# Performance work log

Hardware: AMD Instinct MI355X
Metric: run time of the kernel (lower is better)

Reference implementation:

```python
import jax, jax.numpy as jnp
import numpy as np

B, T, C = 4, 2048, 1024
H = 16
HD = C // H  # 64


def setup_inputs() -> dict:
    key = jax.random.key(0)
    ks = jax.random.split(key, 4)
    x = jax.random.normal(ks[0], (B, T, C), dtype=jnp.float32)
    # c_attn: Linear(C, 3C, bias=False)  (qkv_bias=False)
    w_attn = jax.random.normal(ks[1], (C, 3 * C), dtype=jnp.float32) / np.sqrt(C)
    # c_proj: Linear(C, C) with bias (nn.Linear default)
    w_proj = jax.random.normal(ks[2], (C, C), dtype=jnp.float32) / np.sqrt(C)
    b_proj = jax.random.normal(ks[3], (C,), dtype=jnp.float32) * 0.01
    return {"x": x, "w_attn": w_attn, "w_proj": w_proj, "b_proj": b_proj}


def reference(x, w_attn, w_proj, b_proj):
    b, t, c = x.shape
    qkv = x @ w_attn  # [B,T,3C]
    q, k, v = jnp.split(qkv, 3, axis=-1)
    # [B,H,T,HD]
    q = q.reshape(b, t, H, HD).transpose(0, 2, 1, 3)
    k = k.reshape(b, t, H, HD).transpose(0, 2, 1, 3)
    v = v.reshape(b, t, H, HD).transpose(0, 2, 1, 3)
    scale = 1.0 / np.sqrt(HD)
    attn = jnp.einsum('bhqd,bhkd->bhqk', q, k) * scale  # [B,H,T,T]
    causal = jnp.tril(jnp.ones((t, t), dtype=bool))
    attn = jnp.where(causal, attn, -jnp.inf)
    attn = jax.nn.softmax(attn, axis=-1)
    out = jnp.einsum('bhqk,bhkd->bhqd', attn, v)  # [B,H,T,HD]
    out = out.transpose(0, 2, 1, 3).reshape(b, t, c)
    return out @ w_proj + b_proj
```

## Files before the change

kernel.cpp:

```cpp
#include <hip/hip_runtime.h>

#define BB 4
#define TT 2048
#define CC 1024
#define C3 3072
#define HH 16
#define HD 64
#define BT 8192

#define TS 32
#define TSZ (64 * TS)

typedef __bf16 bf16x8 __attribute__((ext_vector_type(8)));
typedef float floatx4 __attribute__((ext_vector_type(4)));
typedef unsigned uintx2 __attribute__((ext_vector_type(2)));
typedef unsigned short u16;

__device__ __forceinline__ u16 f2bf(float f) {
  union { float f; unsigned u; } a; a.f = f;
  return (u16)((a.u + 0x7fffu + ((a.u >> 16) & 1u)) >> 16);
}
__device__ __forceinline__ bf16x8 ld8(const u16* p) { return *(const bf16x8*)p; }
__device__ __forceinline__ floatx4 mfma16(bf16x8 a, bf16x8 b, floatx4 c) {
  return __builtin_amdgcn_mfma_f32_16x16x32_bf16(a, b, c, 0, 0, 0);
}

__device__ __forceinline__ void gload16(const u16* g, u16* l) {
  __builtin_amdgcn_global_load_lds(
      (const __attribute__((address_space(1))) void*)g,
      (__attribute__((address_space(3))) void*)l, 16, 0, 0);
}

__device__ __forceinline__ void qd_xchg(unsigned a, unsigned b,
                                        unsigned& r0, unsigned& r1) {
  uintx2 t = __builtin_amdgcn_permlane32_swap(a, b, false, false);
  uintx2 r = __builtin_amdgcn_permlane16_swap(t[0], t[1], false, false);
  r0 = r[0]; r1 = r[1];
}

__global__ __launch_bounds__(256) void tobf16_kernel(const float4* __restrict__ src,
                                                     ushort4* __restrict__ dst, int n4) {
  int i = blockIdx.x * 256 + threadIdx.x;
  if (i >= n4) return;
  float4 v = src[i];
  ushort4 o; o.x = f2bf(v.x); o.y = f2bf(v.y); o.z = f2bf(v.z); o.w = f2bf(v.w);
  dst[i] = o;
}

__global__ __launch_bounds__(256) void transpose_bf16_kernel(const float* __restrict__ src,
                                                             u16* __restrict__ dst,
                                                             int K, int N) {
  __shared__ float s[64][65];
  const int t = threadIdx.x;
  const int r = t >> 4;
  const int c = (t & 15) * 4;
  const int k0 = blockIdx.y * 64, n0 = blockIdx.x * 64;
#pragma unroll
  for (int i = 0; i < 4; ++i) {
    float4 v = *(const float4*)&src[(size_t)(k0 + r + i * 16) * N + n0 + c];
    s[r + i * 16][c + 0] = v.x; s[r + i * 16][c + 1] = v.y;
    s[r + i * 16][c + 2] = v.z; s[r + i * 16][c + 3] = v.w;
  }
  __syncthreads();
#pragma unroll
  for (int i = 0; i < 4; ++i) {
    const int nn = r + i * 16;
    ushort4 o;
    o.x = f2bf(s[c + 0][nn]); o.y = f2bf(s[c + 1][nn]);
    o.z = f2bf(s[c + 2][nn]); o.w = f2bf(s[c + 3][nn]);
    *(ushort4*)&dst[(size_t)(n0 + nn) * K + k0 + c] = o;
  }
}

template<int MODE>
__global__ __launch_bounds__(256) void gemm_kernel(
    const u16* __restrict__ A, const u16* __restrict__ B,
    const float* __restrict__ bias, float* __restrict__ outf,
    u16* __restrict__ qk, u16* __restrict__ vT,
    int M, int N, int K) {
  __shared__ u16 smem[2][2][2 * TSZ];

  const int t = threadIdx.x;
  const int w = t >> 6, lane = t & 63, lr = lane & 15, qd = lane >> 4;
  const int wm = w >> 1, wn = w & 1;
  const int m0 = blockIdx.y * 128, n0 = blockIdx.x * 128;

  const int sr = t >> 2;
  const int sc = (t & 3) * 8;
  const int wb = (t & ~63) * 8;
  const u16* Ag = A + (size_t)(m0 + sr) * K + sc;
  const u16* Bg = B + (size_t)(n0 + sr) * K + sc;

  floatx4 acc[4][4] = {};

  {
    u16* sA = &smem[0][0][0];
    u16* sB = &smem[0][1][0];
    gload16(Ag,                  &sA[wb]);
    gload16(Ag + (size_t)64 * K, &sA[TSZ + wb]);
    gload16(Bg,                  &sB[wb]);
    gload16(Bg + (size_t)64 * K, &sB[TSZ + wb]);
  }
  __syncthreads();

  for (int k0 = 0; k0 < K; k0 += 32) {
    const int p = (k0 >> 5) & 1;
    if (k0 + 32 < K) {
      u16* sA = &smem[p ^ 1][0][0];
      u16* sB = &smem[p ^ 1][1][0];
      gload16(Ag + k0 + 32,                  &sA[wb]);
      gload16(Ag + (size_t)64 * K + k0 + 32, &sA[TSZ + wb]);
      gload16(Bg + k0 + 32,                  &sB[wb]);
      gload16(Bg + (size_t)64 * K + k0 + 32, &sB[TSZ + wb]);
    }
    const u16* sA = &smem[p][0][0];
    const u16* sB = &smem[p][1][0];

    bf16x8 af[4], bf[4];
#pragma unroll
    for (int mj = 0; mj < 4; ++mj) af[mj] = ld8(&sA[(wm * 64 + mj * 16 + lr) * TS + qd * 8]);
#pragma unroll
    for (int nj = 0; nj < 4; ++nj) bf[nj] = ld8(&sB[(wn * 64 + nj * 16 + lr) * TS + qd * 8]);
#pragma unroll
    for (int mj = 0; mj < 4; ++mj)
#pragma unroll
      for (int nj = 0; nj < 4; ++nj)
        acc[mj][nj] = mfma16(af[mj], bf[nj], acc[mj][nj]);
    __syncthreads();
  }

  const int rowg0 = m0 + wm * 64;
  const int colg0 = n0 + wn * 64;
  if constexpr (MODE == 2) {
#pragma unroll
    for (int nj = 0; nj < 4; ++nj) {
      const int col = colg0 + nj * 16 + lr;
      const float bv = bias[col];
#pragma unroll
      for (int mj = 0; mj < 4; ++mj)
#pragma unroll
        for (int i = 0; i < 4; ++i)
          outf[(size_t)(rowg0 + mj * 16 + qd * 4 + i) * N + col] = acc[mj][nj][i] + bv;
    }
  } else {
    u16* Tw = &smem[0][0][0] + w * (32 * 72);
    const bool isV = (n0 >= 2 * CC);
    if (!isV) {
      const float qs = (n0 < CC) ? 0.18033688011f : 1.0f;
#pragma unroll
      for (int half = 0; half < 2; ++half) {
#pragma unroll
        for (int m2 = 0; m2 < 2; ++m2)
#pragma unroll
          for (int nj = 0; nj < 4; ++nj)
#pragma unroll
            for (int i = 0; i < 4; ++i)
              Tw[(m2 * 16 + qd * 4 + i) * 72 + nj * 16 + lr] =
                  f2bf(acc[half * 2 + m2][nj][i] * qs);
#pragma unroll
        for (int s = 0; s < 4; ++s) {
          const int rl = s * 8 + (lane >> 3);
          const int c0 = (lane & 7) * 8;
          *(bf16x8*)&qk[(size_t)(rowg0 + half * 32 + rl) * (2 * CC) + colg0 + c0] =
              ld8(&Tw[rl * 72 + c0]);
        }
      }
    } else {
      const int bI = m0 >> 11;
      const int tbase = (m0 & (TT - 1)) + wm * 64;
      const int dim0 = colg0 - 2 * CC;
#pragma unroll
      for (int half = 0; half < 2; ++half) {
#pragma unroll
        for (int n2 = 0; n2 < 2; ++n2)
#pragma unroll
          for (int mj = 0; mj < 4; ++mj)
#pragma unroll
            for (int i = 0; i < 4; ++i)
              Tw[(n2 * 16 + lr) * 72 + mj * 16 + qd * 4 + i] =
                  f2bf(acc[mj][half * 2 + n2][i]);
#pragma unroll
        for (int s = 0; s < 4; ++s) {
          const int dl = s * 8 + (lane >> 3);
          const int t0 = (lane & 7) * 8;
          *(bf16x8*)&vT[((size_t)(bI << 10) + dim0 + half * 32 + dl) * TT + tbase + t0] =
              ld8(&Tw[dl * 72 + t0]);
        }
      }
    }
  }
}

__global__ __launch_bounds__(256, 5) void attn_kernel(const u16* __restrict__ qk,
                                                      const u16* __restrict__ vT,
                                                      u16* __restrict__ att) {
  __shared__ u16 sKV[2][4][TSZ];

  const int t = threadIdx.x;
  const int w = t >> 6, lane = t & 63, lr = lane & 15, qd = lane >> 4;
  const int qtile = 31 - blockIdx.y;
  const int bh = blockIdx.x;
  const int b = bh >> 4, h = bh & 15;
  const int q0 = qtile * 64;
  const u16* qbase = qk + (size_t)b * TT * (2 * CC);

  const u16* qp = qbase + (size_t)(q0 + w * 16 + lr) * (2 * CC) + h * HD;
  const bf16x8 qf0 = ld8(qp + qd * 8);
  const bf16x8 qf1 = ld8(qp + 32 + qd * 8);

  const int sr = t >> 2, sc = (t & 3) * 8;
  const int wb = (t & ~63) * 8;
  const u16* Kg = qbase + (size_t)sr * (2 * CC) + CC + h * HD + sc;
  const u16* Vg = vT + ((size_t)bh * HD + sr) * TT + sc;

  float lsum = 0.f;
  floatx4 o[4] = {};
  const int myq = q0 + w * 16 + lr;

  {
    u16* b0 = &sKV[0][0][0];
    gload16(Kg,      &b0[wb]);
    gload16(Kg + 32, &b0[TSZ + wb]);
    gload16(Vg,      &b0[2 * TSZ + wb]);
    gload16(Vg + 32, &b0[3 * TSZ + wb]);
  }
  __syncthreads();

  for (int kt = 0; kt <= qtile; ++kt) {
    if (kt < qtile) {
      const int kn = (kt + 1) * 64;
      u16* bn = &sKV[(kt + 1) & 1][0][0];
      gload16(Kg + (size_t)kn * (2 * CC),      &bn[wb]);
      gload16(Kg + (size_t)kn * (2 * CC) + 32, &bn[TSZ + wb]);
      gload16(Vg + kn,                         &bn[2 * TSZ + wb]);
      gload16(Vg + kn + 32,                    &bn[3 * TSZ + wb]);
    }

    const u16* sK0 = &sKV[kt & 1][0][0];
    const u16* sK1 = &sKV[kt & 1][1][0];
    const u16* sV0 = &sKV[kt & 1][2][0];
    const u16* sV1 = &sKV[kt & 1][3][0];

    floatx4 s[4] = {};
#pragma unroll
    for (int j = 0; j < 4; ++j) {
      bf16x8 kf0 = ld8(&sK0[(j * 16 + lr) * TS + qd * 8]);
      bf16x8 kf1 = ld8(&sK1[(j * 16 + lr) * TS + qd * 8]);
      s[j] = mfma16(kf0, qf0, s[j]);
      s[j] = mfma16(kf1, qf1, s[j]);
    }

    const bool diag = (kt == qtile);
    unsigned W[4][2];
#pragma unroll
    for (int j = 0; j < 4; ++j) {
      float p[4];
#pragma unroll
      for (int i = 0; i < 4; ++i) {
        p[i] = __builtin_amdgcn_exp2f(s[j][i]);
        if (diag) {
          const int key = kt * 64 + j * 16 + qd * 4 + i;
          p[i] = (key <= myq) ? p[i] : 0.f;
        }
        lsum += p[i];
      }
      W[j][0] = __builtin_amdgcn_perm(__float_as_uint(p[1]), __float_as_uint(p[0]), 0x07060302);
      W[j][1] = __builtin_amdgcn_perm(__float_as_uint(p[3]), __float_as_uint(p[2]), 0x07060302);
    }

    uint4 F0, F1;
    qd_xchg(W[0][0], W[1][0], F0.x, F0.z);
    qd_xchg(W[0][1], W[1][1], F0.y, F0.w);
    qd_xchg(W[2][0], W[3][0], F1.x, F1.z);
    qd_xchg(W[2][1], W[3][1], F1.y, F1.w);
    const bf16x8 pf0 = __builtin_bit_cast(bf16x8, F0);
    const bf16x8 pf1 = __builtin_bit_cast(bf16x8, F1);

#pragma unroll
    for (int j = 0; j < 4; ++j) {
      bf16x8 vf0 = ld8(&sV0[(j * 16 + lr) * TS + qd * 8]);
      bf16x8 vf1 = ld8(&sV1[(j * 16 + lr) * TS + qd * 8]);
      o[j] = mfma16(pf0, vf0, o[j]);
      o[j] = mfma16(pf1, vf1, o[j]);
    }
    __syncthreads();
  }

  lsum += __shfl_xor(lsum, 16);
  lsum += __shfl_xor(lsum, 32);
  float linv[4];
#pragma unroll
  for (int i = 0; i < 4; ++i) linv[i] = 1.0f / __shfl(lsum, qd * 4 + i);

#pragma unroll
  for (int j = 0; j < 4; ++j)
#pragma unroll
    for (int i = 0; i < 4; ++i) {
      const size_t row = (size_t)b * TT + q0 + w * 16 + qd * 4 + i;
      att[row * CC + h * HD + j * 16 + lr] = f2bf(o[j][i] * linv[i]);
    }
}

extern "C" void kernel_launch(void* const* d_in, const int* in_sizes, int n_in,
                              void* d_out, int out_size, void* d_ws, size_t ws_size,
                              hipStream_t stream) {
  const float* x      = (const float*)d_in[0];
  const float* w_attn = (const float*)d_in[1];
  const float* w_proj = (const float*)d_in[2];
  const float* b_proj = (const float*)d_in[3];
  float* out = (float*)d_out;

  char* ws = (char*)d_ws;
  u16* xb  = (u16*)(ws + 0);
  u16* waT = (u16*)(ws + 16777216);
  u16* wpT = (u16*)(ws + 23068672);
  u16* qk  = (u16*)(ws + 25165824);
  u16* vT  = (u16*)(ws + 58720256);
  u16* att = (u16*)(ws + 75497472);

  tobf16_kernel<<<8192, 256, 0, stream>>>((const float4*)x, (ushort4*)xb, 2097152);
  transpose_bf16_kernel<<<dim3(48, 16), 256, 0, stream>>>(w_attn, waT, CC, C3);
  transpose_bf16_kernel<<<dim3(16, 16), 256, 0, stream>>>(w_proj, wpT, CC, CC);

  gemm_kernel<1><<<dim3(24, 64), 256, 0, stream>>>(xb, waT, nullptr, nullptr, qk, vT,
                                                   BT, C3, CC);
  attn_kernel<<<dim3(64, 32), 256, 0, stream>>>(qk, vT, att);

  gemm_kernel<2><<<dim3(8, 64), 256, 0, stream>>>(att, wpT, b_proj, out, nullptr, nullptr,
                                                  BT, CC, CC);
}
```

Before: 236.2 us.

## Split attention key tile across warp pairs and reduce partial outputs in LDS

Each warp now handles 32 query rows and half of each 64-key tile, instead of 16 query rows and the full tile. K and V fragments loaded from shared memory are therefore reused across two query subtiles, which cuts LDS reads per MFMA. The partial outputs and row sums from the two key halves are combined through shared memory in a final reduction. The cost is more registers (launch bounds drop to 4 blocks per SM) plus one extra sync and LDS round trip at the end.

```diff
diff --git a/kernel.cpp b/kernel.cpp
--- a/kernel.cpp
+++ b/kernel.cpp
@@ -191,31 +191,39 @@
   }
 }
 
-__global__ __launch_bounds__(256, 5) void attn_kernel(const u16* __restrict__ qk,
+__global__ __launch_bounds__(256, 4) void attn_kernel(const u16* __restrict__ qk,
                                                       const u16* __restrict__ vT,
                                                       u16* __restrict__ att) {
   __shared__ u16 sKV[2][4][TSZ];
 
   const int t = threadIdx.x;
   const int w = t >> 6, lane = t & 63, lr = lane & 15, qd = lane >> 4;
+  const int m2 = w >> 1;
+  const int ks = w & 1;
   const int qtile = 31 - blockIdx.y;
   const int bh = blockIdx.x;
   const int b = bh >> 4, h = bh & 15;
   const int q0 = qtile * 64;
   const u16* qbase = qk + (size_t)b * TT * (2 * CC);
 
-  const u16* qp = qbase + (size_t)(q0 + w * 16 + lr) * (2 * CC) + h * HD;
-  const bf16x8 qf0 = ld8(qp + qd * 8);
-  const bf16x8 qf1 = ld8(qp + 32 + qd * 8);
+  bf16x8 qf[2][2];
+  int myq[2];
+#pragma unroll
+  for (int ms = 0; ms < 2; ++ms) {
+    const int qrow = q0 + m2 * 32 + ms * 16 + lr;
+    myq[ms] = qrow;
+    const u16* qp = qbase + (size_t)qrow * (2 * CC) + h * HD;
+    qf[ms][0] = ld8(qp + qd * 8);
+    qf[ms][1] = ld8(qp + 32 + qd * 8);
+  }
 
   const int sr = t >> 2, sc = (t & 3) * 8;
   const int wb = (t & ~63) * 8;
   const u16* Kg = qbase + (size_t)sr * (2 * CC) + CC + h * HD + sc;
   const u16* Vg = vT + ((size_t)bh * HD + sr) * TT + sc;
 
-  float lsum = 0.f;
-  floatx4 o[4] = {};
-  const int myq = q0 + w * 16 + lr;
+  float lsum[2] = {0.f, 0.f};
+  floatx4 o[2][4] = {};
 
   {
     u16* b0 = &sKV[0][0][0];
@@ -238,67 +246,99 @@
 
     const u16* sK0 = &sKV[kt & 1][0][0];
     const u16* sK1 = &sKV[kt & 1][1][0];
-    const u16* sV0 = &sKV[kt & 1][2][0];
-    const u16* sV1 = &sKV[kt & 1][3][0];
-
-    floatx4 s[4] = {};
+    const u16* sVk = &sKV[kt & 1][2 + ks][0];
+
+    floatx4 s[2][2] = {};
+#pragma unroll
+    for (int ku = 0; ku < 2; ++ku) {
+      const int krow = ks * 32 + ku * 16 + lr;
+      bf16x8 kf0 = ld8(&sK0[krow * TS + qd * 8]);
+      bf16x8 kf1 = ld8(&sK1[krow * TS + qd * 8]);
+#pragma unroll
+      for (int ms = 0; ms < 2; ++ms) {
+        s[ms][ku] = mfma16(kf0, qf[ms][0], s[ms][ku]);
+        s[ms][ku] = mfma16(kf1, qf[ms][1], s[ms][ku]);
+      }
+    }
+
+    const bool diag = (kt == qtile);
+    uint4 F[2];
+#pragma unroll
+    for (int ms = 0; ms < 2; ++ms) {
+      unsigned W[2][2];
+#pragma unroll
+      for (int ku = 0; ku < 2; ++ku) {
+        float p[4];
+#pragma unroll
+        for (int i = 0; i < 4; ++i) {
+          p[i] = __builtin_amdgcn_exp2f(s[ms][ku][i]);
+          if (diag) {
+            const int key = kt * 64 + ks * 32 + ku * 16 + qd * 4 + i;
+            p[i] = (key <= myq[ms]) ? p[i] : 0.f;
+          }
+          lsum[ms] += p[i];
+        }
+        W[ku][0] = __builtin_amdgcn_perm(__float_as_uint(p[1]), __float_as_uint(p[0]), 0x07060302);
+        W[ku][1] = __builtin_amdgcn_perm(__float_as_uint(p[3]), __float_as_uint(p[2]), 0x07060302);
+      }
+      qd_xchg(W[0][0], W[1][0], F[ms].x, F[ms].z);
+      qd_xchg(W[0][1], W[1][1], F[ms].y, F[ms].w);
+    }
+    const bf16x8 pf0 = __builtin_bit_cast(bf16x8, F[0]);
+    const bf16x8 pf1 = __builtin_bit_cast(bf16x8, F[1]);
+
 #pragma unroll
     for (int j = 0; j < 4; ++j) {
-      bf16x8 kf0 = ld8(&sK0[(j * 16 + lr) * TS + qd * 8]);
-      bf16x8 kf1 = ld8(&sK1[(j * 16 + lr) * TS + qd * 8]);
-      s[j] = mfma16(kf0, qf0, s[j]);
-      s[j] = mfma16(kf1, qf1, s[j]);
-    }
-
-    const bool diag = (kt == qtile);
-    unsigned W[4][2];
-#pragma unroll
-    for (int j = 0; j < 4; ++j) {
-      float p[4];
-#pragma unroll
-      for (int i = 0; i < 4; ++i) {
-        p[i] = __builtin_amdgcn_exp2f(s[j][i]);
-        if (diag) {
-          const int key = kt * 64 + j * 16 + qd * 4 + i;
-          p[i] = (key <= myq) ? p[i] : 0.f;
+      bf16x8 vf = ld8(&sVk[(j * 16 + lr) * TS + qd * 8]);
+      o[0][j] = mfma16(pf0, vf, o[0][j]);
+      o[1][j] = mfma16(pf1, vf, o[1][j]);
+    }
+    __syncthreads();
+  }
+
+#pragma unroll
+  for (int ms = 0; ms < 2; ++ms) {
+    lsum[ms] += __shfl_xor(lsum[ms], 16);
+    lsum[ms] += __shfl_xor(lsum[ms], 32);
+  }
+
+  float* sO = (float*)&sKV[0][0][0];
+  float* sL = (float*)((char*)&sKV[0][0][0] + 17408);
+
+  if (qd == 0) {
+    sL[w * 32 + lr]      = lsum[0];
+    sL[w * 32 + 16 + lr] = lsum[1];
+  }
+  if (ks == 1) {
+#pragma unroll
+    for (int ms = 0; ms < 2; ++ms)
+#pragma unroll
+      for (int j = 0; j < 4; ++j)
+#pragma unroll
+        for (int i = 0; i < 4; ++i)
+          sO[(m2 * 32 + ms * 16 + qd * 4 + i) * 68 + j * 16 + lr] = o[ms][j][i];
+  }
+  __syncthreads();
+
+  if (ks == 0) {
+    const int pw = w + 1;
+#pragma unroll
+    for (int ms = 0; ms < 2; ++ms) {
+      const float lt = lsum[ms] + sL[pw * 32 + ms * 16 + lr];
+      float linv[4];
+#pragma unroll
+      for (int i = 0; i < 4; ++i) linv[i] = 1.0f / __shfl(lt, qd * 4 + i);
+#pragma unroll
+      for (int j = 0; j < 4; ++j)
+#pragma unroll
+        for (int i = 0; i < 4; ++i) {
+          const float ov = o[ms][j][i] +
+              sO[(m2 * 32 + ms * 16 + qd * 4 + i) * 68 + j * 16 + lr];
+          const size_t row = (size_t)b * TT + q0 + m2 * 32 + ms * 16 + qd * 4 + i;
+          att[row * CC + h * HD + j * 16 + lr] = f2bf(ov * linv[i]);
         }
-        lsum += p[i];
-      }
-      W[j][0] = __builtin_amdgcn_perm(__float_as_uint(p[1]), __float_as_uint(p[0]), 0x07060302);
-      W[j][1] = __builtin_amdgcn_perm(__float_as_uint(p[3]), __float_as_uint(p[2]), 0x07060302);
-    }
-
-    uint4 F0, F1;
-    qd_xchg(W[0][0], W[1][0], F0.x, F0.z);
-    qd_xchg(W[0][1], W[1][1], F0.y, F0.w);
-    qd_xchg(W[2][0], W[3][0], F1.x, F1.z);
-    qd_xchg(W[2][1], W[3][1], F1.y, F1.w);
-    const bf16x8 pf0 = __builtin_bit_cast(bf16x8, F0);
-    const bf16x8 pf1 = __builtin_bit_cast(bf16x8, F1);
-
-#pragma unroll
-    for (int j = 0; j < 4; ++j) {
-      bf16x8 vf0 = ld8(&sV0[(j * 16 + lr) * TS + qd * 8]);
-      bf16x8 vf1 = ld8(&sV1[(j * 16 + lr) * TS + qd * 8]);
-      o[j] = mfma16(pf0, vf0, o[j]);
-      o[j] = mfma16(pf1, vf1, o[j]);
-    }
-    __syncthreads();
-  }
-
-  lsum += __shfl_xor(lsum, 16);
-  lsum += __shfl_xor(lsum, 32);
-  float linv[4];
-#pragma unroll
-  for (int i = 0; i < 4; ++i) linv[i] = 1.0f / __shfl(lsum, qd * 4 + i);
-
-#pragma unroll
-  for (int j = 0; j < 4; ++j)
-#pragma unroll
-    for (int i = 0; i < 4; ++i) {
-      const size_t row = (size_t)b * TT + q0 + w * 16 + qd * 4 + i;
-      att[row * CC + h * HD + j * 16 + lr] = f2bf(o[j][i] * linv[i]);
-    }
+    }
+  }
 }
 
 extern "C" void kernel_launch(void* const* d_in, const int* in_sizes, int n_in,
```

After: 237.9 us. No clear change (+0.7%).

## Replace QKV GEMM with 256x256-tile 8-wave kernel using swizzled LDS pipeline

Applied to the files above, without the earlier changes.

Adds a new QKV projection GEMM that gives each 512-thread block a 256x256 output tile with K-step 64. It uses XOR-swizzled LDS staging through direct global-to-LDS loads, and a hand-scheduled eight-phase loop that interleaves loads for later K tiles with MFMA phases, gated by vmcnt waits and raw barriers. The larger tile raises data reuse per byte loaded and is meant to hide memory latency, with setprio favouring the MFMA bursts. The cost is more accumulator registers and a fragile manual schedule that hard-codes K=1024 (8 iterations of 2 K-tiles). The old MODE 1 path is removed from the generic GEMM, which now only serves the output projection.

```diff
diff --git a/kernel.cpp b/kernel.cpp
--- a/kernel.cpp
+++ b/kernel.cpp
@@ -37,6 +37,11 @@
   uintx2 r = __builtin_amdgcn_permlane16_swap(t[0], t[1], false, false);
   r0 = r[0]; r1 = r[1];
 }
+
+#define BARR do { asm volatile("" ::: "memory"); \
+                  __builtin_amdgcn_s_barrier(); \
+                  asm volatile("" ::: "memory"); } while (0)
+#define VMW4 asm volatile("s_waitcnt vmcnt(4)" ::: "memory")
 
 __global__ __launch_bounds__(256) void tobf16_kernel(const float4* __restrict__ src,
                                                      ushort4* __restrict__ dst, int n4) {
@@ -72,11 +77,136 @@
   }
 }
 
+__global__ __launch_bounds__(512, 2) void gemm256_kernel(
+    const u16* __restrict__ A, const u16* __restrict__ B,
+    u16* __restrict__ qk, u16* __restrict__ vT, int K) {
+  __shared__ u16 lds[2][2][2][8192];
+
+  const int t = threadIdx.x;
+  const int lane = t & 63, lr = lane & 15, qd = lane >> 4;
+  const int w = t >> 6, wm2 = w >> 2, wn4 = w & 3;
+  const int m0 = blockIdx.y * 256, n0 = blockIdx.x * 256;
+
+  const int srow = t >> 3;
+  const int scol = ((t & 7) ^ (srow & 7)) * 8;
+  const u16* Asrc = A + (size_t)(m0 + srow) * K + scol;
+  const u16* Bsrc = B + (size_t)(n0 + srow) * K + scol;
+  const int wvb = (t & ~63) * 8;
+
+  const int NT = K >> 6;
+  floatx4 acc[8][4] = {};
+
+  const int lr64 = lr * 64;
+  const int csw0 = (qd * 8) ^ ((lr & 7) * 8);
+  const int csw1 = (32 + qd * 8) ^ ((lr & 7) * 8);
+
+#define STG(PR, MT, HF, TK) do { if ((TK) < NT) { \
+    const u16* g_ = ((MT) ? Bsrc : Asrc) + (size_t)((HF) * 128) * K + (TK) * 64; \
+    u16* l_ = &lds[PR][MT][HF][wvb]; \
+    gload16(g_, l_); \
+    gload16(g_ + (size_t)64 * K, l_ + 4096); } } while (0)
+
+#define PHASE(PR, MQ, NQ) do { \
+    const u16* As_ = &lds[PR][0][MQ][0]; \
+    const u16* Bs_ = &lds[PR][1][NQ][0]; \
+    bf16x8 af_[4][2], bf_[2][2]; \
+    _Pragma("unroll") \
+    for (int mi = 0; mi < 4; ++mi) { \
+      const int rb = (wm2 * 64 + mi * 16) * 64 + lr64; \
+      af_[mi][0] = ld8(&As_[rb + csw0]); af_[mi][1] = ld8(&As_[rb + csw1]); } \
+    _Pragma("unroll") \
+    for (int ni = 0; ni < 2; ++ni) { \
+      const int rb = (wn4 * 32 + ni * 16) * 64 + lr64; \
+      bf_[ni][0] = ld8(&Bs_[rb + csw0]); bf_[ni][1] = ld8(&Bs_[rb + csw1]); } \
+    __builtin_amdgcn_s_setprio(1); \
+    _Pragma("unroll") \
+    for (int mi = 0; mi < 4; ++mi) \
+      _Pragma("unroll") \
+      for (int ni = 0; ni < 2; ++ni) { \
+        acc[(MQ)*4+mi][(NQ)*2+ni] = mfma16(af_[mi][0], bf_[ni][0], acc[(MQ)*4+mi][(NQ)*2+ni]); \
+        acc[(MQ)*4+mi][(NQ)*2+ni] = mfma16(af_[mi][1], bf_[ni][1], acc[(MQ)*4+mi][(NQ)*2+ni]); } \
+    __builtin_amdgcn_s_setprio(0); \
+  } while (0)
+
+  STG(0, 0, 0, 0); STG(0, 1, 0, 0); STG(0, 0, 1, 0); STG(0, 1, 1, 0);
+  STG(1, 1, 0, 1); STG(1, 0, 0, 1);
+  VMW4; BARR;
+
+  for (int it = 0; it < 8; ++it) {
+    const int To = 2 * it + 1, Tn = 2 * it + 2, Tm = 2 * it + 3;
+    STG(1, 0, 1, To); STG(1, 1, 1, To); PHASE(0, 0, 0);       BARR;
+    PHASE(0, 1, 0);                                            BARR;
+    STG(0, 1, 0, Tn); PHASE(0, 0, 1);                          BARR;
+    STG(0, 0, 0, Tn); PHASE(0, 1, 1);                    VMW4; BARR;
+    STG(0, 0, 1, Tn); PHASE(1, 0, 0);                          BARR;
+    STG(0, 1, 1, Tn); PHASE(1, 1, 0);                          BARR;
+    STG(1, 1, 0, Tm); PHASE(1, 0, 1);                          BARR;
+    STG(1, 0, 0, Tm); PHASE(1, 1, 1);                    VMW4; BARR;
+  }
+#undef STG
+#undef PHASE
+
+  const bool isV = (n0 >= 2 * CC);
+  if (!isV) {
+    const float qs = (n0 < CC) ? 0.18033688011f : 1.0f;
+    u16* Tw = ((u16*)&lds[0][0][0][0]) + w * (32 * 40);
+#pragma unroll
+    for (int mq = 0; mq < 2; ++mq)
+#pragma unroll
+      for (int mi2 = 0; mi2 < 2; ++mi2)
+#pragma unroll
+        for (int nq = 0; nq < 2; ++nq) {
+#pragma unroll
+          for (int mh = 0; mh < 2; ++mh)
+#pragma unroll
+            for (int ni = 0; ni < 2; ++ni)
+#pragma unroll
+              for (int i = 0; i < 4; ++i)
+                Tw[(mh * 16 + qd * 4 + i) * 40 + ni * 16 + lr] =
+                    f2bf(acc[mq * 4 + mi2 * 2 + mh][nq * 2 + ni][i] * qs);
+          const int R0 = m0 + mq * 128 + wm2 * 64 + mi2 * 32;
+          const int C0 = n0 + nq * 128 + wn4 * 32;
+#pragma unroll
+          for (int s = 0; s < 2; ++s) {
+            const int rl = s * 16 + (lane >> 2);
+            const int c0 = (lane & 3) * 8;
+            *(bf16x8*)&qk[(size_t)(R0 + rl) * (2 * CC) + C0 + c0] =
+                ld8(&Tw[rl * 40 + c0]);
+          }
+        }
+  } else {
+    u16* Tv = ((u16*)&lds[0][0][0][0]) + w * (32 * 72);
+    const int bI = m0 >> 11;
+#pragma unroll
+    for (int mq = 0; mq < 2; ++mq) {
+      const int tbase = (m0 & (TT - 1)) + mq * 128 + wm2 * 64;
+#pragma unroll
+      for (int nq = 0; nq < 2; ++nq) {
+        const int dim0 = (n0 - 2 * CC) + nq * 128 + wn4 * 32;
+#pragma unroll
+        for (int ni = 0; ni < 2; ++ni)
+#pragma unroll
+          for (int mi = 0; mi < 4; ++mi)
+#pragma unroll
+            for (int i = 0; i < 4; ++i)
+              Tv[(ni * 16 + lr) * 72 + mi * 16 + qd * 4 + i] =
+                  f2bf(acc[mq * 4 + mi][nq * 2 + ni][i]);
+#pragma unroll
+        for (int s = 0; s < 4; ++s) {
+          const int dl = s * 8 + (lane >> 3);
+          const int t0 = (lane & 7) * 8;
+          *(bf16x8*)&vT[((size_t)(bI << 10) + dim0 + dl) * TT + tbase + t0] =
+              ld8(&Tv[dl * 72 + t0]);
+        }
+      }
+    }
+  }
+}
+
 template<int MODE>
 __global__ __launch_bounds__(256) void gemm_kernel(
     const u16* __restrict__ A, const u16* __restrict__ B,
     const float* __restrict__ bias, float* __restrict__ outf,
-    u16* __restrict__ qk, u16* __restrict__ vT,
     int M, int N, int K) {
   __shared__ u16 smem[2][2][2 * TSZ];
 
@@ -131,63 +261,15 @@
 
   const int rowg0 = m0 + wm * 64;
   const int colg0 = n0 + wn * 64;
-  if constexpr (MODE == 2) {
-#pragma unroll
-    for (int nj = 0; nj < 4; ++nj) {
-      const int col = colg0 + nj * 16 + lr;
-      const float bv = bias[col];
-#pragma unroll
-      for (int mj = 0; mj < 4; ++mj)
-#pragma unroll
-        for (int i = 0; i < 4; ++i)
-          outf[(size_t)(rowg0 + mj * 16 + qd * 4 + i) * N + col] = acc[mj][nj][i] + bv;
-    }
-  } else {
-    u16* Tw = &smem[0][0][0] + w * (32 * 72);
-    const bool isV = (n0 >= 2 * CC);
-    if (!isV) {
-      const float qs = (n0 < CC) ? 0.18033688011f : 1.0f;
-#pragma unroll
-      for (int half = 0; half < 2; ++half) {
-#pragma unroll
-        for (int m2 = 0; m2 < 2; ++m2)
-#pragma unroll
-          for (int nj = 0; nj < 4; ++nj)
-#pragma unroll
-            for (int i = 0; i < 4; ++i)
-              Tw[(m2 * 16 + qd * 4 + i) * 72 + nj * 16 + lr] =
-                  f2bf(acc[half * 2 + m2][nj][i] * qs);
-#pragma unroll
-        for (int s = 0; s < 4; ++s) {
-          const int rl = s * 8 + (lane >> 3);
-          const int c0 = (lane & 7) * 8;
-          *(bf16x8*)&qk[(size_t)(rowg0 + half * 32 + rl) * (2 * CC) + colg0 + c0] =
-              ld8(&Tw[rl * 72 + c0]);
-        }
-      }
-    } else {
-      const int bI = m0 >> 11;
-      const int tbase = (m0 & (TT - 1)) + wm * 64;
-      const int dim0 = colg0 - 2 * CC;
-#pragma unroll
-      for (int half = 0; half < 2; ++half) {
-#pragma unroll
-        for (int n2 = 0; n2 < 2; ++n2)
-#pragma unroll
-          for (int mj = 0; mj < 4; ++mj)
-#pragma unroll
-            for (int i = 0; i < 4; ++i)
-              Tw[(n2 * 16 + lr) * 72 + mj * 16 + qd * 4 + i] =
-                  f2bf(acc[mj][half * 2 + n2][i]);
-#pragma unroll
-        for (int s = 0; s < 4; ++s) {
-          const int dl = s * 8 + (lane >> 3);
-          const int t0 = (lane & 7) * 8;
-          *(bf16x8*)&vT[((size_t)(bI << 10) + dim0 + half * 32 + dl) * TT + tbase + t0] =
-              ld8(&Tw[dl * 72 + t0]);
-        }
-      }
-    }
+#pragma unroll
+  for (int nj = 0; nj < 4; ++nj) {
+    const int col = colg0 + nj * 16 + lr;
+    const float bv = bias[col];
+#pragma unroll
+    for (int mj = 0; mj < 4; ++mj)
+#pragma unroll
+      for (int i = 0; i < 4; ++i)
+        outf[(size_t)(rowg0 + mj * 16 + qd * 4 + i) * N + col] = acc[mj][nj][i] + bv;
   }
 }
 
@@ -322,10 +404,10 @@
   transpose_bf16_kernel<<<dim3(48, 16), 256, 0, stream>>>(w_attn, waT, CC, C3);
   transpose_bf16_kernel<<<dim3(16, 16), 256, 0, stream>>>(w_proj, wpT, CC, CC);
 
-  gemm_kernel<1><<<dim3(24, 64), 256, 0, stream>>>(xb, waT, nullptr, nullptr, qk, vT,
-                                                   BT, C3, CC);
+  gemm256_kernel<<<dim3(12, 32), 512, 0, stream>>>(xb, waT, qk, vT, CC);
+
   attn_kernel<<<dim3(64, 32), 256, 0, stream>>>(qk, vT, att);
 
-  gemm_kernel<2><<<dim3(8, 64), 256, 0, stream>>>(att, wpT, b_proj, out, nullptr, nullptr,
+  gemm_kernel<2><<<dim3(8, 64), 256, 0, stream>>>(att, wpT, b_proj, out,
                                                   BT, CC, CC);
 }
```

New measurement: 234.3 us. Within noise of the previous version (-0.8%).

## Rewrite GEMM as 256x128 tile, 512-thread kernel with swizzled LDS and split-phase pipeline

Applied to the files above, without the earlier changes.

Replaces the 128x128, 256-thread GEMM with a 256x128 tile handled by 8 waves at K-step 64. LDS gets an XOR swizzle to avoid bank conflicts, and loads are staged in phases with explicit vmcnt waits and raw barriers so global-to-LDS copies overlap with the MFMA work. MFMA sections run at raised priority. The aim is better operand reuse and latency hiding for both projection GEMMs, at the cost of fewer blocks and tighter register and LDS pressure.

```diff
diff --git a/kernel.cpp b/kernel.cpp
--- a/kernel.cpp
+++ b/kernel.cpp
@@ -37,6 +37,12 @@
   uintx2 r = __builtin_amdgcn_permlane16_swap(t[0], t[1], false, false);
   r0 = r[0]; r1 = r[1];
 }
+
+#define BARR do { asm volatile("" ::: "memory"); \
+                  __builtin_amdgcn_s_barrier(); \
+                  asm volatile("" ::: "memory"); } while (0)
+#define VMW4 asm volatile("s_waitcnt vmcnt(4)" ::: "memory")
+#define VMW0 asm volatile("s_waitcnt vmcnt(0)" ::: "memory")
 
 __global__ __launch_bounds__(256) void tobf16_kernel(const float4* __restrict__ src,
                                                      ushort4* __restrict__ dst, int n4) {
@@ -73,119 +79,139 @@
 }
 
 template<int MODE>
-__global__ __launch_bounds__(256) void gemm_kernel(
+__global__ __launch_bounds__(512, 2) void gemm256_kernel(
     const u16* __restrict__ A, const u16* __restrict__ B,
     const float* __restrict__ bias, float* __restrict__ outf,
-    u16* __restrict__ qk, u16* __restrict__ vT,
-    int M, int N, int K) {
-  __shared__ u16 smem[2][2][2 * TSZ];
+    u16* __restrict__ qk, u16* __restrict__ vT, int N, int K) {
+  __shared__ u16 lds[2][24576];
 
   const int t = threadIdx.x;
-  const int w = t >> 6, lane = t & 63, lr = lane & 15, qd = lane >> 4;
-  const int wm = w >> 1, wn = w & 1;
-  const int m0 = blockIdx.y * 128, n0 = blockIdx.x * 128;
-
-  const int sr = t >> 2;
-  const int sc = (t & 3) * 8;
-  const int wb = (t & ~63) * 8;
-  const u16* Ag = A + (size_t)(m0 + sr) * K + sc;
-  const u16* Bg = B + (size_t)(n0 + sr) * K + sc;
-
+  const int lane = t & 63, lr = lane & 15, qd = lane >> 4;
+  const int w = t >> 6, wm = w >> 1, wn = w & 1;
+  const int m0 = blockIdx.y * 256, n0 = blockIdx.x * 128;
+
+  const int srow = t >> 3;
+  const int scol = ((t & 7) ^ (srow & 7)) * 8;
+  const u16* Asrc = A + (size_t)(m0 + srow) * K + scol;
+  const u16* Bsrc = B + (size_t)(n0 + srow) * K + scol;
+  const int wvb = (t & ~63) * 8;
+
+  const int NT = K >> 6;
   floatx4 acc[4][4] = {};
 
-  {
-    u16* sA = &smem[0][0][0];
-    u16* sB = &smem[0][1][0];
-    gload16(Ag,                  &sA[wb]);
-    gload16(Ag + (size_t)64 * K, &sA[TSZ + wb]);
-    gload16(Bg,                  &sB[wb]);
-    gload16(Bg + (size_t)64 * K, &sB[TSZ + wb]);
-  }
-  __syncthreads();
-
-  for (int k0 = 0; k0 < K; k0 += 32) {
-    const int p = (k0 >> 5) & 1;
-    if (k0 + 32 < K) {
-      u16* sA = &smem[p ^ 1][0][0];
-      u16* sB = &smem[p ^ 1][1][0];
-      gload16(Ag + k0 + 32,                  &sA[wb]);
-      gload16(Ag + (size_t)64 * K + k0 + 32, &sA[TSZ + wb]);
-      gload16(Bg + k0 + 32,                  &sB[wb]);
-      gload16(Bg + (size_t)64 * K + k0 + 32, &sB[TSZ + wb]);
-    }
-    const u16* sA = &smem[p][0][0];
-    const u16* sB = &smem[p][1][0];
-
-    bf16x8 af[4], bf[4];
-#pragma unroll
-    for (int mj = 0; mj < 4; ++mj) af[mj] = ld8(&sA[(wm * 64 + mj * 16 + lr) * TS + qd * 8]);
-#pragma unroll
-    for (int nj = 0; nj < 4; ++nj) bf[nj] = ld8(&sB[(wn * 64 + nj * 16 + lr) * TS + qd * 8]);
-#pragma unroll
-    for (int mj = 0; mj < 4; ++mj)
-#pragma unroll
-      for (int nj = 0; nj < 4; ++nj)
-        acc[mj][nj] = mfma16(af[mj], bf[nj], acc[mj][nj]);
-    __syncthreads();
-  }
-
-  const int rowg0 = m0 + wm * 64;
-  const int colg0 = n0 + wn * 64;
+  const int abase = (wm * 64 + lr) * 64;
+  const int bbase = (wn * 64 + lr) * 64;
+  const int csw0 = (qd * 8) ^ ((lr & 7) * 8);
+  const int csw1 = (32 + qd * 8) ^ ((lr & 7) * 8);
+
+#define STG_A(PR, QA, TK) do { if ((TK) < NT) \
+    gload16(Asrc + (size_t)((QA) * 64) * K + (TK) * 64, \
+            &lds[PR][(QA) * 4096 + wvb]); } while (0)
+#define STG_B(PR, HB, TK) do { if ((TK) < NT) \
+    gload16(Bsrc + (size_t)((HB) * 64) * K + (TK) * 64, \
+            &lds[PR][16384 + (HB) * 4096 + wvb]); } while (0)
+
+  bf16x8 af[4][2], bf[2][2];
+#define READ_A(PR) do { _Pragma("unroll") for (int mi = 0; mi < 4; ++mi) { \
+    const u16* p_ = &lds[PR][mi * 1024 + abase]; \
+    af[mi][0] = ld8(p_ + csw0); af[mi][1] = ld8(p_ + csw1); } } while (0)
+#define READ_B(PR, NJ0) do { _Pragma("unroll") for (int nj = 0; nj < 2; ++nj) { \
+    const u16* p_ = &lds[PR][16384 + ((NJ0) + nj) * 1024 + bbase]; \
+    bf[nj][0] = ld8(p_ + csw0); bf[nj][1] = ld8(p_ + csw1); } } while (0)
+#define MFMA16(NJ0) do { __builtin_amdgcn_s_setprio(1); _Pragma("unroll") \
+    for (int mi = 0; mi < 4; ++mi) _Pragma("unroll") for (int nj = 0; nj < 2; ++nj) { \
+      acc[mi][(NJ0) + nj] = mfma16(af[mi][0], bf[nj][0], acc[mi][(NJ0) + nj]); \
+      acc[mi][(NJ0) + nj] = mfma16(af[mi][1], bf[nj][1], acc[mi][(NJ0) + nj]); } \
+    __builtin_amdgcn_s_setprio(0); } while (0)
+
+  STG_A(0, 0, 0); STG_A(0, 1, 0); STG_A(0, 2, 0); STG_A(0, 3, 0);
+  STG_B(0, 0, 0); STG_B(0, 1, 0);
+  STG_A(1, 0, 1); STG_A(1, 1, 1); STG_A(1, 2, 1); STG_A(1, 3, 1);
+  VMW4; BARR;
+
+  const int NITER = NT >> 1;
+  for (int it = 0; it < NITER; ++it) {
+    const int T1 = 2 * it + 1, T2 = 2 * it + 2, T3 = 2 * it + 3;
+    const bool last = (it == NITER - 1);
+    STG_B(1, 0, T1); STG_B(1, 1, T1);
+    READ_A(0); READ_B(0, 0); MFMA16(0);
+    BARR;
+    STG_A(0, 0, T2); STG_A(0, 1, T2); STG_A(0, 2, T2); STG_A(0, 3, T2);
+    READ_B(0, 2); MFMA16(2);
+    if (last) { VMW0; } else { VMW4; }
+    BARR;
+    STG_B(0, 0, T2); STG_B(0, 1, T2);
+    READ_A(1); READ_B(1, 0); MFMA16(0);
+    BARR;
+    STG_A(1, 0, T3); STG_A(1, 1, T3); STG_A(1, 2, T3); STG_A(1, 3, T3);
+    READ_B(1, 2); MFMA16(2);
+    if (last) { VMW0; } else { VMW4; }
+    BARR;
+  }
+#undef STG_A
+#undef STG_B
+#undef READ_A
+#undef READ_B
+#undef MFMA16
+
+  u16* flat = &lds[0][0];
   if constexpr (MODE == 2) {
+    const int rowg0 = m0 + wm * 64;
+    const int colg0 = n0 + wn * 64;
 #pragma unroll
     for (int nj = 0; nj < 4; ++nj) {
       const int col = colg0 + nj * 16 + lr;
       const float bv = bias[col];
 #pragma unroll
-      for (int mj = 0; mj < 4; ++mj)
+      for (int mi = 0; mi < 4; ++mi)
 #pragma unroll
         for (int i = 0; i < 4; ++i)
-          outf[(size_t)(rowg0 + mj * 16 + qd * 4 + i) * N + col] = acc[mj][nj][i] + bv;
+          outf[(size_t)(rowg0 + mi * 16 + qd * 4 + i) * N + col] = acc[mi][nj][i] + bv;
     }
   } else {
-    u16* Tw = &smem[0][0][0] + w * (32 * 72);
     const bool isV = (n0 >= 2 * CC);
     if (!isV) {
       const float qs = (n0 < CC) ? 0.18033688011f : 1.0f;
-#pragma unroll
-      for (int half = 0; half < 2; ++half) {
-#pragma unroll
-        for (int m2 = 0; m2 < 2; ++m2)
+      u16* Tw = flat + w * (32 * 72);
+      const int C0 = n0 + wn * 64;
+#pragma unroll
+      for (int mi2 = 0; mi2 < 2; ++mi2) {
+#pragma unroll
+        for (int mh = 0; mh < 2; ++mh)
 #pragma unroll
           for (int nj = 0; nj < 4; ++nj)
 #pragma unroll
             for (int i = 0; i < 4; ++i)
-              Tw[(m2 * 16 + qd * 4 + i) * 72 + nj * 16 + lr] =
-                  f2bf(acc[half * 2 + m2][nj][i] * qs);
+              Tw[(mh * 16 + qd * 4 + i) * 72 + nj * 16 + lr] =
+                  f2bf(acc[mi2 * 2 + mh][nj][i] * qs);
+        const int R0 = m0 + wm * 64 + mi2 * 32;
 #pragma unroll
         for (int s = 0; s < 4; ++s) {
           const int rl = s * 8 + (lane >> 3);
           const int c0 = (lane & 7) * 8;
-          *(bf16x8*)&qk[(size_t)(rowg0 + half * 32 + rl) * (2 * CC) + colg0 + c0] =
+          *(bf16x8*)&qk[(size_t)(R0 + rl) * (2 * CC) + C0 + c0] =
               ld8(&Tw[rl * 72 + c0]);
         }
       }
     } else {
+      u16* Tv = flat + w * (64 * 72);
       const int bI = m0 >> 11;
       const int tbase = (m0 & (TT - 1)) + wm * 64;
-      const int dim0 = colg0 - 2 * CC;
-#pragma unroll
-      for (int half = 0; half < 2; ++half) {
-#pragma unroll
-        for (int n2 = 0; n2 < 2; ++n2)
-#pragma unroll
-          for (int mj = 0; mj < 4; ++mj)
-#pragma unroll
-            for (int i = 0; i < 4; ++i)
-              Tw[(n2 * 16 + lr) * 72 + mj * 16 + qd * 4 + i] =
-                  f2bf(acc[mj][half * 2 + n2][i]);
-#pragma unroll
-        for (int s = 0; s < 4; ++s) {
-          const int dl = s * 8 + (lane >> 3);
-          const int t0 = (lane & 7) * 8;
-          *(bf16x8*)&vT[((size_t)(bI << 10) + dim0 + half * 32 + dl) * TT + tbase + t0] =
-              ld8(&Tw[dl * 72 + t0]);
-        }
+      const int dim0 = (n0 - 2 * CC) + wn * 64;
+#pragma unroll
+      for (int nj = 0; nj < 4; ++nj)
+#pragma unroll
+        for (int mi = 0; mi < 4; ++mi)
+#pragma unroll
+          for (int i = 0; i < 4; ++i)
+            Tv[(nj * 16 + lr) * 72 + mi * 16 + qd * 4 + i] =
+                f2bf(acc[mi][nj][i]);
+#pragma unroll
+      for (int s = 0; s < 8; ++s) {
+        const int dl = s * 8 + (lane >> 3);
+        const int t0 = (lane & 7) * 8;
+        *(bf16x8*)&vT[((size_t)(bI << 10) + dim0 + dl) * TT + tbase + t0] =
+            ld8(&Tv[dl * 72 + t0]);
       }
     }
   }
@@ -322,10 +348,11 @@
   transpose_bf16_kernel<<<dim3(48, 16), 256, 0, stream>>>(w_attn, waT, CC, C3);
   transpose_bf16_kernel<<<dim3(16, 16), 256, 0, stream>>>(w_proj, wpT, CC, CC);
 
-  gemm_kernel<1><<<dim3(24, 64), 256, 0, stream>>>(xb, waT, nullptr, nullptr, qk, vT,
-                                                   BT, C3, CC);
+  gemm256_kernel<1><<<dim3(24, 32), 512, 0, stream>>>(xb, waT, nullptr, nullptr,
+                                                      qk, vT, C3, CC);
+
   attn_kernel<<<dim3(64, 32), 256, 0, stream>>>(qk, vT, att);
 
-  gemm_kernel<2><<<dim3(8, 64), 256, 0, stream>>>(att, wpT, b_proj, out, nullptr, nullptr,
-                                                  BT, CC, CC);
-}
+  gemm256_kernel<2><<<dim3(8, 32), 512, 0, stream>>>(att, wpT, b_proj, out,
+                                                     nullptr, nullptr, CC, CC);
+}
```

Result: no change. 232.6 us (-1.6%).
